# Optimization experiments

Hardware: AMD Instinct MI355X
Metric: run time of the kernel (lower is better)

Reference implementation:

```python
import jax, jax.numpy as jnp
import numpy as np

HIDDEN_DIM = 1000
CONTEXT_DIM = 2000


def setup_inputs() -> dict:
    key = jax.random.key(0)
    k1, k2, k3, k4 = jax.random.split(key, 4)
    B, N = 64, 1024
    std = 0.001
    return {
        "s_prev": jax.random.normal(k1, (B, HIDDEN_DIM), dtype=jnp.float32),
        "h_j": jax.random.normal(k2, (B, N, CONTEXT_DIM), dtype=jnp.float32),
        "W_a": jax.random.normal(k3, (HIDDEN_DIM, HIDDEN_DIM), dtype=jnp.float32) * std,
        "U_a": jax.random.normal(k4, (HIDDEN_DIM, CONTEXT_DIM), dtype=jnp.float32) * std,
        "v_a": jnp.zeros((HIDDEN_DIM,), dtype=jnp.float32),
    }


def reference(s_prev, h_j, W_a, U_a, v_a):
    # W_a s: (B, H); U_a h: (B, N, H)
    W_a_s = jnp.einsum("bd,hd->bh", s_prev, W_a)
    U_a_h = jnp.einsum("bnc,hc->bnh", h_j, U_a)
    energy = jnp.tanh(W_a_s[:, None, :] + U_a_h)  # (B, N, H)
    scores = jnp.einsum("bnh,h->bn", energy, v_a)  # (B, N)
    return scores
```

## Files before the change

### kernel.cpp

```cpp
#include <hip/hip_runtime.h>
#include <hip/hip_bf16.h>

#define HID 1000
#define CTX 2000
#define KP   2016
#define HP   1024
#define BATCH 64
#define NSEQ 1024
#define M_TOT (BATCH * NSEQ)
#define WSTR 1024

typedef __attribute__((ext_vector_type(8))) short short8;
typedef __attribute__((ext_vector_type(4))) float floatx4;

__device__ __forceinline__ unsigned short f2bf(float x) {
    union { float f; unsigned u; } v; v.f = x;
    unsigned r = v.u + 0x7FFFu + ((v.u >> 16) & 1u);
    return (unsigned short)(r >> 16);
}

typedef const __attribute__((address_space(1))) unsigned glb_u32;
typedef __attribute__((address_space(3))) unsigned lds_u32;
__device__ __forceinline__ void gload16(const void* g, void* l) {
    __builtin_amdgcn_global_load_lds((glb_u32*)g, (lds_u32*)l, 16, 0, 0);
}

__global__ void zero_kernel(float* __restrict__ out, int n) {
    int i = blockIdx.x * 256 + threadIdx.x;
    if (i < n) out[i] = 0.0f;
}

__global__ void convertA_kernel(const float* __restrict__ src, unsigned short* __restrict__ dst) {
    int row = blockIdx.x;
    int t = threadIdx.x;
    if (t >= KP / 8) return;
    unsigned short pk[8];
    if (t < CTX / 8) {
        const float* p = src + (size_t)row * CTX + t * 8;
        float4 a = *(const float4*)p;
        float4 b = *(const float4*)(p + 4);
        pk[0]=f2bf(a.x); pk[1]=f2bf(a.y); pk[2]=f2bf(a.z); pk[3]=f2bf(a.w);
        pk[4]=f2bf(b.x); pk[5]=f2bf(b.y); pk[6]=f2bf(b.z); pk[7]=f2bf(b.w);
    } else {
#pragma unroll
        for (int i = 0; i < 8; i++) pk[i] = 0;
    }
    *(short8*)(dst + (size_t)row * KP + t * 8) = *(short8*)pk;
}

__global__ void convertB_kernel(const float* __restrict__ src, unsigned short* __restrict__ dst) {
    int row = blockIdx.x;
    int t = threadIdx.x;
    if (t >= KP / 8) return;
    unsigned short pk[8];
    if (row < HID && t < CTX / 8) {
        const float* p = src + (size_t)row * CTX + t * 8;
        float4 a = *(const float4*)p;
        float4 b = *(const float4*)(p + 4);
        pk[0]=f2bf(a.x); pk[1]=f2bf(a.y); pk[2]=f2bf(a.z); pk[3]=f2bf(a.w);
        pk[4]=f2bf(b.x); pk[5]=f2bf(b.y); pk[6]=f2bf(b.z); pk[7]=f2bf(b.w);
    } else {
#pragma unroll
        for (int i = 0; i < 8; i++) pk[i] = 0;
    }
    *(short8*)(dst + (size_t)row * KP + t * 8) = *(short8*)pk;
}

__global__ void ws_kernel(const float* __restrict__ s_prev,
                          const float* __restrict__ W_a,
                          float* __restrict__ W_s) {
    int wave = threadIdx.x >> 6, lane = threadIdx.x & 63;
    int gw = blockIdx.x * 4 + wave;
    int b = gw / HID, h = gw % HID;
    const float* wr = W_a + (size_t)h * HID;
    const float* sr = s_prev + (size_t)b * HID;
    float acc = 0.0f;
#pragma unroll
    for (int it = 0; it < 4; ++it) {
        int idx = it * 64 + lane;
        if (idx < HID / 4) {
            float4 w = *(const float4*)(wr + idx * 4);
            float4 s = *(const float4*)(sr + idx * 4);
            acc += w.x * s.x + w.y * s.y + w.z * s.z + w.w * s.w;
        }
    }
    acc += __shfl_xor(acc, 1);
    acc += __shfl_xor(acc, 2);
    acc += __shfl_xor(acc, 4);
    acc += __shfl_xor(acc, 8);
    acc += __shfl_xor(acc, 16);
    acc += __shfl_xor(acc, 32);
    if (lane == 0) W_s[b * WSTR + h] = acc;
}

__global__ __launch_bounds__(256, 2) void gemm_kernel(
        const unsigned short* __restrict__ A, const unsigned short* __restrict__ B,
        const float* __restrict__ W_s, const float* __restrict__ v_a,
        float* __restrict__ out) {
    __shared__ __align__(16) unsigned short As[128 * 32];
    __shared__ __align__(16) unsigned short Bs[128 * 32];

    const int tid  = threadIdx.x;
    const int lane = tid & 63;
    const int wave = tid >> 6;
    const int wm = wave & 1, wh = wave >> 1;
    const int ln = lane & 15, quad = lane >> 4;

    const int m0 = blockIdx.x * 128;
    const int b  = m0 >> 10;

    const int srow = lane >> 2;
    const int scol = (lane & 3) * 8;
    const unsigned short* abase0 = A + (size_t)(m0 + wave * 16 + srow) * KP + scol;
    const unsigned short* abase1 = abase0 + (size_t)64 * KP;
    unsigned short* asl0 = &As[(wave * 16) * 32];
    unsigned short* asl1 = &As[(64 + wave * 16) * 32];
    unsigned short* bsl0 = &Bs[(wave * 16) * 32];
    unsigned short* bsl1 = &Bs[(64 + wave * 16) * 32];

    float rowsum[4][4];
#pragma unroll
    for (int i = 0; i < 4; i++)
#pragma unroll
        for (int r = 0; r < 4; r++) rowsum[i][r] = 0.0f;

    for (int ht = 0; ht < HP / 128; ++ht) {
        const unsigned short* aptr0 = abase0;
        const unsigned short* aptr1 = abase1;
        const unsigned short* bptr0 = B + (size_t)(ht * 128 + wave * 16 + srow) * KP + scol;
        const unsigned short* bptr1 = bptr0 + (size_t)64 * KP;

        floatx4 acc[4][4];
#pragma unroll
        for (int i = 0; i < 4; i++)
#pragma unroll
            for (int j = 0; j < 4; j++) acc[i][j] = (floatx4)0.0f;

        for (int kk = 0; kk < KP / 32; ++kk) {
            __syncthreads();
            gload16(aptr0, asl0);
            gload16(aptr1, asl1);
            gload16(bptr0, bsl0);
            gload16(bptr1, bsl1);
            aptr0 += 32; aptr1 += 32; bptr0 += 32; bptr1 += 32;
            __syncthreads();

            short8 af[4], bfr[4];
#pragma unroll
            for (int i = 0; i < 4; i++)
                af[i] = *(const short8*)&As[(wm * 64 + i * 16 + ln) * 32 + quad * 8];
#pragma unroll
            for (int j = 0; j < 4; j++)
                bfr[j] = *(const short8*)&Bs[(wh * 64 + j * 16 + ln) * 32 + quad * 8];
#pragma unroll
            for (int i = 0; i < 4; i++)
#pragma unroll
                for (int j = 0; j < 4; j++)
                    acc[i][j] = __builtin_amdgcn_mfma_f32_16x16x32_bf16(af[i], bfr[j], acc[i][j], 0, 0, 0);
        }

#pragma unroll
        for (int j = 0; j < 4; j++) {
            const int h = ht * 128 + wh * 64 + j * 16 + ln;
            float wsv = 0.0f, vav = 0.0f;
            if (h < HID) { wsv = W_s[b * WSTR + h]; vav = v_a[h]; }
#pragma unroll
            for (int i = 0; i < 4; i++)
#pragma unroll
                for (int r = 0; r < 4; r++)
                    rowsum[i][r] += vav * tanhf(acc[i][j][r] + wsv);
        }
    }

#pragma unroll
    for (int i = 0; i < 4; i++)
#pragma unroll
        for (int r = 0; r < 4; r++) {
            float v = rowsum[i][r];
            v += __shfl_xor(v, 1);
            v += __shfl_xor(v, 2);
            v += __shfl_xor(v, 4);
            v += __shfl_xor(v, 8);
            rowsum[i][r] = v;
        }

    if (ln == 0) {
#pragma unroll
        for (int i = 0; i < 4; i++) {
            const int row = m0 + wm * 64 + i * 16 + quad * 4;
#pragma unroll
            for (int r = 0; r < 4; r++)
                atomicAdd(&out[row + r], rowsum[i][r]);
        }
    }
}

extern "C" void kernel_launch(void* const* d_in, const int* in_sizes, int n_in,
                              void* d_out, int out_size, void* d_ws, size_t ws_size,
                              hipStream_t stream) {
    const float* s_prev = (const float*)d_in[0];
    const float* h_j    = (const float*)d_in[1];
    const float* W_a    = (const float*)d_in[2];
    const float* U_a    = (const float*)d_in[3];
    const float* v_a    = (const float*)d_in[4];
    float* out = (float*)d_out;

    const size_t b_off = 64 * WSTR * sizeof(float);
    const size_t a_off = b_off + (size_t)HP * KP * sizeof(short);
    float* W_s = (float*)d_ws;
    unsigned short* B_bf = (unsigned short*)((char*)d_ws + b_off);
    unsigned short* A_bf = (unsigned short*)((char*)d_ws + a_off);

    zero_kernel<<<dim3(M_TOT / 256), 256, 0, stream>>>(out, M_TOT);
    ws_kernel<<<dim3(BATCH * HID / 4), 256, 0, stream>>>(s_prev, W_a, W_s);
    convertA_kernel<<<dim3(M_TOT), 256, 0, stream>>>(h_j, A_bf);
    convertB_kernel<<<dim3(HP), 256, 0, stream>>>(U_a, B_bf);
    gemm_kernel<<<dim3(M_TOT / 128), 256, 0, stream>>>(A_bf, B_bf, W_s, v_a, out);
}
```

Baseline: 1.195 ms.

## Double-buffer GEMM LDS, split H tiles across blocks, swizzle layout, fast tanh

The GEMM now uses double-buffered LDS tiles so the next K-slice's global-to-LDS load overlaps the MFMA work, with one barrier per iteration instead of two. Each block now owns one H tile rather than looping over all eight, which multiplies the grid by eight and raises the occupancy hint to 4. Block IDs are remapped so that blocks on the same XCD share A rows. The conversion kernels write a column-swizzled layout that is read back with a matching XOR to reduce LDS bank conflicts. tanhf is replaced by an exp-based fast approximation, which may cost some accuracy.

```diff
diff --git a/kernel.cpp b/kernel.cpp
--- a/kernel.cpp
+++ b/kernel.cpp
@@ -25,6 +25,12 @@
     __builtin_amdgcn_global_load_lds((glb_u32*)g, (lds_u32*)l, 16, 0, 0);
 }
 
+__device__ __forceinline__ float fast_tanh(float x) {
+    float cx = fminf(fmaxf(x, -15.f), 15.f);
+    float e = __expf(2.f * cx);
+    return __fdividef(e - 1.f, e + 1.f);
+}
+
 __global__ void zero_kernel(float* __restrict__ out, int n) {
     int i = blockIdx.x * 256 + threadIdx.x;
     if (i < n) out[i] = 0.0f;
@@ -34,9 +40,11 @@
     int row = blockIdx.x;
     int t = threadIdx.x;
     if (t >= KP / 8) return;
+    int pc = t & 3, grp = t >> 2;
+    int sc = (grp << 2) | (pc ^ ((row >> 1) & 3));
     unsigned short pk[8];
-    if (t < CTX / 8) {
-        const float* p = src + (size_t)row * CTX + t * 8;
+    if (sc < CTX / 8) {
+        const float* p = src + (size_t)row * CTX + sc * 8;
         float4 a = *(const float4*)p;
         float4 b = *(const float4*)(p + 4);
         pk[0]=f2bf(a.x); pk[1]=f2bf(a.y); pk[2]=f2bf(a.z); pk[3]=f2bf(a.w);
@@ -52,9 +60,11 @@
     int row = blockIdx.x;
     int t = threadIdx.x;
     if (t >= KP / 8) return;
+    int pc = t & 3, grp = t >> 2;
+    int sc = (grp << 2) | (pc ^ ((row >> 1) & 3));
     unsigned short pk[8];
-    if (row < HID && t < CTX / 8) {
-        const float* p = src + (size_t)row * CTX + t * 8;
+    if (row < HID && sc < CTX / 8) {
+        const float* p = src + (size_t)row * CTX + sc * 8;
         float4 a = *(const float4*)p;
         float4 b = *(const float4*)(p + 4);
         pk[0]=f2bf(a.x); pk[1]=f2bf(a.y); pk[2]=f2bf(a.z); pk[3]=f2bf(a.w);
@@ -93,12 +103,12 @@
     if (lane == 0) W_s[b * WSTR + h] = acc;
 }
 
-__global__ __launch_bounds__(256, 2) void gemm_kernel(
+__global__ __launch_bounds__(256, 4) void gemm_kernel(
         const unsigned short* __restrict__ A, const unsigned short* __restrict__ B,
         const float* __restrict__ W_s, const float* __restrict__ v_a,
         float* __restrict__ out) {
-    __shared__ __align__(16) unsigned short As[128 * 32];
-    __shared__ __align__(16) unsigned short Bs[128 * 32];
+    __shared__ __align__(16) unsigned short As[2 * 128 * 32];
+    __shared__ __align__(16) unsigned short Bs[2 * 128 * 32];
 
     const int tid  = threadIdx.x;
     const int lane = tid & 63;
@@ -106,17 +116,63 @@
     const int wm = wave & 1, wh = wave >> 1;
     const int ln = lane & 15, quad = lane >> 4;
 
-    const int m0 = blockIdx.x * 128;
-    const int b  = m0 >> 10;
-
-    const int srow = lane >> 2;
-    const int scol = (lane & 3) * 8;
+    const int bid = blockIdx.x;
+    const int xcd = bid & 7, seq = bid >> 3;
+    const int m0 = (xcd * 64 + (seq >> 3)) * 128;
+    const int ht = seq & 7;
+    const int bb = m0 >> 10;
+
+    const int srow = lane >> 2, scol = (lane & 3) * 8;
     const unsigned short* abase0 = A + (size_t)(m0 + wave * 16 + srow) * KP + scol;
     const unsigned short* abase1 = abase0 + (size_t)64 * KP;
-    unsigned short* asl0 = &As[(wave * 16) * 32];
-    unsigned short* asl1 = &As[(64 + wave * 16) * 32];
-    unsigned short* bsl0 = &Bs[(wave * 16) * 32];
-    unsigned short* bsl1 = &Bs[(64 + wave * 16) * 32];
+    const unsigned short* bbase0 = B + (size_t)(ht * 128 + wave * 16 + srow) * KP + scol;
+    const unsigned short* bbase1 = bbase0 + (size_t)64 * KP;
+    const int sl0 = (wave * 16) * 32;
+    const int sl1 = (64 + wave * 16) * 32;
+
+    const int rsw = ((ln >> 1) & 3) * 8;
+
+    floatx4 acc[4][4];
+#pragma unroll
+    for (int i = 0; i < 4; i++)
+#pragma unroll
+        for (int j = 0; j < 4; j++) acc[i][j] = (floatx4)0.0f;
+
+    gload16(abase0, As + sl0);
+    gload16(abase1, As + sl1);
+    gload16(bbase0, Bs + sl0);
+    gload16(bbase1, Bs + sl1);
+    __syncthreads();
+
+    int p = 0;
+    for (int kk = 0; kk < 63; ++kk) {
+        if (kk < 62) {
+            const int g = (kk + 1) * 32;
+            const int d = ((p ^ 1) << 12);
+            gload16(abase0 + g, As + d + sl0);
+            gload16(abase1 + g, As + d + sl1);
+            gload16(bbase0 + g, Bs + d + sl0);
+            gload16(bbase1 + g, Bs + d + sl1);
+        }
+
+        const unsigned short* ap_ = As + (p << 12);
+        const unsigned short* bp_ = Bs + (p << 12);
+        short8 af[4], bfr[4];
+#pragma unroll
+        for (int i = 0; i < 4; i++)
+            af[i] = *(const short8*)&ap_[(wm * 64 + i * 16 + ln) * 32 + (quad * 8 ^ rsw)];
+#pragma unroll
+        for (int j = 0; j < 4; j++)
+            bfr[j] = *(const short8*)&bp_[(wh * 64 + j * 16 + ln) * 32 + (quad * 8 ^ rsw)];
+#pragma unroll
+        for (int i = 0; i < 4; i++)
+#pragma unroll
+            for (int j = 0; j < 4; j++)
+                acc[i][j] = __builtin_amdgcn_mfma_f32_16x16x32_bf16(af[i], bfr[j], acc[i][j], 0, 0, 0);
+
+        __syncthreads();
+        p ^= 1;
+    }
 
     float rowsum[4][4];
 #pragma unroll
@@ -124,52 +180,16 @@
 #pragma unroll
         for (int r = 0; r < 4; r++) rowsum[i][r] = 0.0f;
 
-    for (int ht = 0; ht < HP / 128; ++ht) {
-        const unsigned short* aptr0 = abase0;
-        const unsigned short* aptr1 = abase1;
-        const unsigned short* bptr0 = B + (size_t)(ht * 128 + wave * 16 + srow) * KP + scol;
-        const unsigned short* bptr1 = bptr0 + (size_t)64 * KP;
-
-        floatx4 acc[4][4];
+#pragma unroll
+    for (int j = 0; j < 4; j++) {
+        const int h = ht * 128 + wh * 64 + j * 16 + ln;
+        float wsv = 0.0f, vav = 0.0f;
+        if (h < HID) { wsv = W_s[bb * WSTR + h]; vav = v_a[h]; }
 #pragma unroll
         for (int i = 0; i < 4; i++)
 #pragma unroll
-            for (int j = 0; j < 4; j++) acc[i][j] = (floatx4)0.0f;
-
-        for (int kk = 0; kk < KP / 32; ++kk) {
-            __syncthreads();
-            gload16(aptr0, asl0);
-            gload16(aptr1, asl1);
-            gload16(bptr0, bsl0);
-            gload16(bptr1, bsl1);
-            aptr0 += 32; aptr1 += 32; bptr0 += 32; bptr1 += 32;
-            __syncthreads();
-
-            short8 af[4], bfr[4];
-#pragma unroll
-            for (int i = 0; i < 4; i++)
-                af[i] = *(const short8*)&As[(wm * 64 + i * 16 + ln) * 32 + quad * 8];
-#pragma unroll
-            for (int j = 0; j < 4; j++)
-                bfr[j] = *(const short8*)&Bs[(wh * 64 + j * 16 + ln) * 32 + quad * 8];
-#pragma unroll
-            for (int i = 0; i < 4; i++)
-#pragma unroll
-                for (int j = 0; j < 4; j++)
-                    acc[i][j] = __builtin_amdgcn_mfma_f32_16x16x32_bf16(af[i], bfr[j], acc[i][j], 0, 0, 0);
-        }
-
-#pragma unroll
-        for (int j = 0; j < 4; j++) {
-            const int h = ht * 128 + wh * 64 + j * 16 + ln;
-            float wsv = 0.0f, vav = 0.0f;
-            if (h < HID) { wsv = W_s[b * WSTR + h]; vav = v_a[h]; }
-#pragma unroll
-            for (int i = 0; i < 4; i++)
-#pragma unroll
-                for (int r = 0; r < 4; r++)
-                    rowsum[i][r] += vav * tanhf(acc[i][j][r] + wsv);
-        }
+            for (int r = 0; r < 4; r++)
+                rowsum[i][r] += vav * fast_tanh(acc[i][j][r] + wsv);
     }
 
 #pragma unroll
@@ -215,5 +235,5 @@
     ws_kernel<<<dim3(BATCH * HID / 4), 256, 0, stream>>>(s_prev, W_a, W_s);
     convertA_kernel<<<dim3(M_TOT), 256, 0, stream>>>(h_j, A_bf);
     convertB_kernel<<<dim3(HP), 256, 0, stream>>>(U_a, B_bf);
-    gemm_kernel<<<dim3(M_TOT / 128), 256, 0, stream>>>(A_bf, B_bf, W_s, v_a, out);
-}
+    gemm_kernel<<<dim3((M_TOT / 128) * (HP / 128)), 256, 0, stream>>>(A_bf, B_bf, W_s, v_a, out);
+}
```

Result: faster. 1.131 ms (-5.4%).
